# Performance work log

Measured on AMD Instinct MI355X. Metric: run time of the kernel, lower is better.

The kernel has to match this reference:

```python
import jax, jax.numpy as jnp
import numpy as np

D_MODEL = 1024
LAYER_IDX = 5
D_FF = 4096
SPARSITY = 0.9
TOKENS = 8192
IN_UP = D_MODEL * (LAYER_IDX + 1)  # 6144


def _sparse_weight(rng, out_f, in_f, sparsity):
    """Row-wise k-sparse weight matrix mimicking SparseLinear's padded-CSR:
    each output row keeps k = round(in_f*(1-sparsity)) live columns,
    values ~ U(-b, b) with b = 1/sqrt(effective_fan_in)."""
    k = max(1, round(in_f * (1.0 - sparsity)))
    bound = 1.0 / np.sqrt(max(1.0, in_f * (1.0 - sparsity)))
    scores = rng.random((out_f, in_f))
    # top-k per row -> boolean mask
    thresh = np.partition(scores, in_f - k, axis=1)[:, in_f - k][:, None]
    mask = scores >= thresh
    W = (rng.uniform(-bound, bound, (out_f, in_f)).astype(np.float32)) * mask
    return jnp.asarray(W), jnp.asarray(mask)


def setup_inputs() -> dict:
    key = jax.random.key(0)
    x = jax.random.normal(key, (TOKENS, IN_UP), dtype=jnp.float32)
    rng = np.random.default_rng(0)
    W_up, mask_up = _sparse_weight(rng, D_FF, IN_UP, SPARSITY)
    W_down, mask_down = _sparse_weight(rng, D_MODEL, D_FF, SPARSITY)
    return {"ffn_input_cat": x, "W_up": W_up, "W_down": W_down,
            "mask_up": mask_up, "mask_down": mask_down}


def reference(ffn_input_cat, W_up, W_down, mask_up, mask_down):
    # fc_down(gelu(fc_up(x))); SparseLinear == masked dense linear, no bias.
    # torch F.gelu default is the exact (erf) gelu.
    h = jax.nn.gelu(ffn_input_cat @ (W_up * mask_up).T, approximate=False)  # [T, d_ff]
    return h @ (W_down * mask_down).T  # [T, d_model]
```

## Files before the change

kernel.cpp:

```cpp
#include <hip/hip_runtime.h>
#include <cstdint>
#include <cstddef>

typedef unsigned short u16;
typedef __attribute__((ext_vector_type(8))) short  bf16x8;
typedef __attribute__((ext_vector_type(4))) float  f32x4;
typedef __attribute__((ext_vector_type(4))) unsigned short u16x4;

__device__ __forceinline__ u16 f2bf(float f) {
    unsigned u = __float_as_uint(f);
    unsigned r = (u + 0x7FFFu + ((u >> 16) & 1u)) >> 16;
    return (u16)r;
}

__device__ __forceinline__ void async_lds16(const u16* g, u16* l) {
    __builtin_amdgcn_global_load_lds(
        (const __attribute__((address_space(1))) unsigned int*)g,
        (__attribute__((address_space(3))) unsigned int*)l,
        16, 0, 0);
}

__global__ __launch_bounds__(256) void cvt3_kernel(const float* __restrict__ s0, u16* __restrict__ d0, int n0,
                                                   const float* __restrict__ s1, u16* __restrict__ d1, int n1,
                                                   const float* __restrict__ s2, u16* __restrict__ d2, int n2) {
    const int total = n0 + n1 + n2;
    for (int i = blockIdx.x * 256 + threadIdx.x; i < total; i += gridDim.x * 256) {
        const float* s; u16* d; int j = i;
        if (j < n0)            { s = s0; d = d0; }
        else if (j < n0 + n1)  { s = s1; d = d1; j -= n0; }
        else                   { s = s2; d = d2; j -= n0 + n1; }
        float4 a = ((const float4*)s)[j];
        u16x4 o;
        o[0] = f2bf(a.x); o[1] = f2bf(a.y); o[2] = f2bf(a.z); o[3] = f2bf(a.w);
        ((u16x4*)d)[j] = o;
    }
}

#define KSTEP 32
#define ASZ (256 * KSTEP)

template<bool GELU, typename OutT, int BN>
__global__ __launch_bounds__(512, 2) void gemm_ffn(const u16* __restrict__ A,
                                                   const u16* __restrict__ B,
                                                   OutT* __restrict__ C,
                                                   int K, int lda, int ldb, int ldc) {
    constexpr int NI = BN / 64;
    constexpr int SL = (BN == 256) ? 4 : 3;
    __shared__ __align__(16) u16 sA[4][ASZ];
    __shared__ __align__(16) u16 sB[4][BN * KSTEP];

    const int tid  = threadIdx.x;
    const int wave = tid >> 6;
    const int lane = tid & 63;
    const int quad = lane >> 4;
    const int r16  = lane & 15;

    const int nwg = gridDim.x * gridDim.y;
    int lin = blockIdx.y * gridDim.x + blockIdx.x;
    lin = (lin & 7) * (nwg >> 3) + (lin >> 3);
    const int n0 = (lin % gridDim.x) * BN;
    const int m0 = (lin / gridDim.x) * 256;

    const int wm = (wave >> 2) * 128;
    const int wn = (wave & 3) * (BN / 4);

    const int sr0 = wave * 16 + (lane >> 2);
    const int gc0 = (((lane & 3) ^ ((sr0 >> 1) & 3))) * 8;
    const int ldsw = wave * 512;

    const u16* gA0 = A + (size_t)(m0 + sr0) * lda + gc0;
    const u16* gA1 = gA0 + (size_t)128 * lda;
    const u16* gB0 = B + (size_t)(n0 + sr0) * ldb + gc0;
    const u16* gB1 = gB0 + (size_t)128 * ldb;

#define STAGE(kt, tb) { const int ko_ = (kt) * KSTEP; \
        async_lds16(gA0 + ko_, &sA[tb][ldsw]); \
        async_lds16(gA1 + ko_, &sA[tb][4096 + ldsw]); \
        async_lds16(gB0 + ko_, &sB[tb][ldsw]); \
        if constexpr (BN == 256) async_lds16(gB1 + ko_, &sB[tb][4096 + ldsw]); }

    int oA[8], oB[NI];
#pragma unroll
    for (int i = 0; i < 8; i++) {
        int ra = wm + i * 16 + r16;
        oA[i] = ra * 32 + ((quad ^ ((ra >> 1) & 3)) << 3);
    }
#pragma unroll
    for (int i = 0; i < NI; i++) {
        int rb = wn + i * 16 + r16;
        oB[i] = rb * 32 + ((quad ^ ((rb >> 1) & 3)) << 3);
    }

    f32x4 acc[8][NI] = {};
    const int NT = K / KSTEP;

#define LGKM0 asm volatile("s_waitcnt lgkmcnt(0)" ::: "memory"); __builtin_amdgcn_sched_barrier(0)
#define SBAR  __builtin_amdgcn_sched_barrier(0)
#define VMCNT_STEADY if constexpr (BN == 256) { asm volatile("s_waitcnt vmcnt(8)" ::: "memory"); } \
                     else { asm volatile("s_waitcnt vmcnt(6)" ::: "memory"); }
#define MFMA_Q(mb, AF, BF) \
    __builtin_amdgcn_s_setprio(1); \
    _Pragma("unroll") \
    for (int mi_ = 0; mi_ < 4; mi_++) \
        _Pragma("unroll") \
        for (int ni_ = 0; ni_ < NI; ni_++) \
            acc[(mb) + mi_][ni_] = __builtin_amdgcn_mfma_f32_16x16x32_bf16( \
                AF[mi_], BF[ni_], acc[(mb) + mi_][ni_], 0, 0, 0); \
    __builtin_amdgcn_s_setprio(0); \
    __builtin_amdgcn_sched_barrier(0)

    bf16x8 afA[4], afB[4], bfA[NI], bfB[NI];

    STAGE(0, 0); STAGE(1, 1); STAGE(2, 2);
    VMCNT_STEADY;
    __builtin_amdgcn_s_barrier();
    SBAR;
#pragma unroll
    for (int i = 0; i < 4; i++)  afA[i] = *(const bf16x8*)&sA[0][oA[i]];
#pragma unroll
    for (int i = 0; i < NI; i++) bfA[i] = *(const bf16x8*)&sB[0][oB[i]];
    LGKM0;

#define STEP(T, c, n1, t3, BC, BNx) { \
        int kt3_ = (T) + 3; if (kt3_ >= NT) kt3_ -= NT; \
        STAGE(kt3_, t3); \
        _Pragma("unroll") \
        for (int i = 0; i < 4; i++) afB[i] = *(const bf16x8*)&sA[c][oA[4 + i]]; \
        SBAR; \
        MFMA_Q(0, afA, BC); \
        LGKM0; \
        VMCNT_STEADY; \
        __builtin_amdgcn_s_barrier(); \
        SBAR; \
        _Pragma("unroll") \
        for (int i = 0; i < 4; i++)  afA[i] = *(const bf16x8*)&sA[n1][oA[i]]; \
        _Pragma("unroll") \
        for (int i = 0; i < NI; i++) BNx[i] = *(const bf16x8*)&sB[n1][oB[i]]; \
        SBAR; \
        MFMA_Q(4, afB, BC); \
        LGKM0; \
    }

    for (int t = 0; t < NT; t += 4) {
        STEP(t + 0, 0, 1, 3, bfA, bfB);
        STEP(t + 1, 1, 2, 0, bfB, bfA);
        STEP(t + 2, 2, 3, 1, bfA, bfB);
        STEP(t + 3, 3, 0, 2, bfB, bfA);
    }
    asm volatile("s_waitcnt vmcnt(0)" ::: "memory");

#pragma unroll
    for (int mi = 0; mi < 8; mi++) {
#pragma unroll
        for (int r = 0; r < 4; r++) {
            size_t rowoff = (size_t)(m0 + wm + mi * 16 + quad * 4 + r) * ldc;
#pragma unroll
            for (int ni = 0; ni < NI; ni++) {
                int col = n0 + wn + ni * 16 + r16;
                float v = acc[mi][ni][r];
                if constexpr (GELU)
                    v = 0.5f * v * (1.0f + erff(v * 0.70710678118654752f));
                if constexpr (sizeof(OutT) == 2)
                    ((u16*)C)[rowoff + col] = f2bf(v);
                else
                    ((float*)C)[rowoff + col] = v;
            }
        }
    }
}

extern "C" void kernel_launch(void* const* d_in, const int* in_sizes, int n_in,
                              void* d_out, int out_size, void* d_ws, size_t ws_size,
                              hipStream_t stream) {
    const int T   = 8192;
    const int DIN = 6144;
    const int DFF = 4096;
    const int DM  = 1024;

    const float* x  = (const float*)d_in[0];
    const float* wu = (const float*)d_in[1];
    const float* wd = (const float*)d_in[2];

    u16* xb  = (u16*)d_ws;
    u16* wub = xb  + (size_t)T * DIN;
    u16* wdb = wub + (size_t)DFF * DIN;
    u16* hb  = wdb + (size_t)DM * DFF;

    const int n4x  = T * DIN / 4;
    const int n4wu = DFF * DIN / 4;
    const int n4wd = DM * DFF / 4;
    cvt3_kernel<<<8192, 256, 0, stream>>>(x, xb, n4x, wu, wub, n4wu, wd, wdb, n4wd);

    dim3 g1(DFF / 256, T / 256);
    gemm_ffn<true, u16, 256><<<g1, 512, 0, stream>>>(xb, wub, hb, DIN, DIN, DIN, DFF);

    dim3 g2(DM / 128, T / 256);
    gemm_ffn<false, float, 128><<<g2, 512, 0, stream>>>(hb, wdb, (float*)d_out,
                                                        DFF, DFF, DFF, DM);
}
```

Measured before the change: 888.9 us.

## Restructure GEMM mainloop to double-buffered 64-wide K tiles with quadrant-split MFMA

```diff
diff --git a/kernel.cpp b/kernel.cpp
--- a/kernel.cpp
+++ b/kernel.cpp
@@ -36,18 +36,16 @@
     }
 }
 
-#define KSTEP 32
-#define ASZ (256 * KSTEP)
 
 template<bool GELU, typename OutT, int BN>
-__global__ __launch_bounds__(512, 2) void gemm_ffn(const u16* __restrict__ A,
-                                                   const u16* __restrict__ B,
-                                                   OutT* __restrict__ C,
-                                                   int K, int lda, int ldb, int ldc) {
-    constexpr int NI = BN / 64;
-    constexpr int SL = (BN == 256) ? 4 : 3;
-    __shared__ __align__(16) u16 sA[4][ASZ];
-    __shared__ __align__(16) u16 sB[4][BN * KSTEP];
+__global__ __launch_bounds__(512, 2) void gemm_q(const u16* __restrict__ A,
+                                                 const u16* __restrict__ B,
+                                                 OutT* __restrict__ C,
+                                                 int K, int lda, int ldb, int ldc) {
+    constexpr int NI  = BN / 64;
+    constexpr int NQN = NI / 2;
+    __shared__ __align__(16) u16 sA[2][256 * 64];
+    __shared__ __align__(16) u16 sB[2][BN * 64];
 
     const int tid  = threadIdx.x;
     const int wave = tid >> 6;
@@ -64,90 +62,88 @@
     const int wm = (wave >> 2) * 128;
     const int wn = (wave & 3) * (BN / 4);
 
-    const int sr0 = wave * 16 + (lane >> 2);
-    const int gc0 = (((lane & 3) ^ ((sr0 >> 1) & 3))) * 8;
-    const int ldsw = wave * 512;
+    const int srow = tid >> 3;
+    const int scol = (((tid & 7) ^ (srow & 7)) << 3);
+    const u16* gAs = A + (size_t)(m0 + srow) * lda + scol;
+    const u16* gBs = B + (size_t)(n0 + srow) * ldb + scol;
 
-    const u16* gA0 = A + (size_t)(m0 + sr0) * lda + gc0;
-    const u16* gA1 = gA0 + (size_t)128 * lda;
-    const u16* gB0 = B + (size_t)(n0 + sr0) * ldb + gc0;
-    const u16* gB1 = gB0 + (size_t)128 * ldb;
+#define STAGE_A(dst, kt) { const size_t ko_ = (size_t)(kt) * 64; \
+    _Pragma("unroll") for (int i_ = 0; i_ < 4; i_++) \
+        async_lds16(gAs + (size_t)(i_ * 64) * lda + ko_, (dst) + i_ * 4096 + tid * 8); }
+#define STAGE_B(dst, kt) { const size_t ko_ = (size_t)(kt) * 64; \
+    _Pragma("unroll") for (int i_ = 0; i_ < NI; i_++) \
+        async_lds16(gBs + (size_t)(i_ * 64) * ldb + ko_, (dst) + i_ * 4096 + tid * 8); }
 
-#define STAGE(kt, tb) { const int ko_ = (kt) * KSTEP; \
-        async_lds16(gA0 + ko_, &sA[tb][ldsw]); \
-        async_lds16(gA1 + ko_, &sA[tb][4096 + ldsw]); \
-        async_lds16(gB0 + ko_, &sB[tb][ldsw]); \
-        if constexpr (BN == 256) async_lds16(gB1 + ko_, &sB[tb][4096 + ldsw]); }
+    const int g0 = (quad ^ (r16 & 7)) << 3;
+    const int g1 = g0 ^ 32;
 
-    int oA[8], oB[NI];
-#pragma unroll
-    for (int i = 0; i < 8; i++) {
-        int ra = wm + i * 16 + r16;
-        oA[i] = ra * 32 + ((quad ^ ((ra >> 1) & 3)) << 3);
-    }
-#pragma unroll
-    for (int i = 0; i < NI; i++) {
-        int rb = wn + i * 16 + r16;
-        oB[i] = rb * 32 + ((quad ^ ((rb >> 1) & 3)) << 3);
-    }
+    struct FragT { bf16x8 a[4][2]; bf16x8 b[NQN][2]; };
 
-    f32x4 acc[8][NI] = {};
-    const int NT = K / KSTEP;
+#define READQ(F, Ab, Bb, qmi, qni) { \
+    _Pragma("unroll") for (int i_ = 0; i_ < 4; i_++) { \
+        const int ao_ = (wm + ((qmi) * 4 + i_) * 16 + r16) * 64; \
+        F.a[i_][0] = *(const bf16x8*)&(Ab)[ao_ + g0]; \
+        F.a[i_][1] = *(const bf16x8*)&(Ab)[ao_ + g1]; } \
+    _Pragma("unroll") for (int i_ = 0; i_ < NQN; i_++) { \
+        const int bo_ = (wn + ((qni) * NQN + i_) * 16 + r16) * 64; \
+        F.b[i_][0] = *(const bf16x8*)&(Bb)[bo_ + g0]; \
+        F.b[i_][1] = *(const bf16x8*)&(Bb)[bo_ + g1]; } }
 
 #define LGKM0 asm volatile("s_waitcnt lgkmcnt(0)" ::: "memory"); __builtin_amdgcn_sched_barrier(0)
-#define SBAR  __builtin_amdgcn_sched_barrier(0)
-#define VMCNT_STEADY if constexpr (BN == 256) { asm volatile("s_waitcnt vmcnt(8)" ::: "memory"); } \
-                     else { asm volatile("s_waitcnt vmcnt(6)" ::: "memory"); }
-#define MFMA_Q(mb, AF, BF) \
+#define VM0   asm volatile("s_waitcnt vmcnt(0)"  ::: "memory"); __builtin_amdgcn_sched_barrier(0)
+#define PIN   __builtin_amdgcn_sched_barrier(0)
+#define BARR  __builtin_amdgcn_s_barrier()
+
+#define MFMAQ(q, F) \
     __builtin_amdgcn_s_setprio(1); \
-    _Pragma("unroll") \
-    for (int mi_ = 0; mi_ < 4; mi_++) \
-        _Pragma("unroll") \
-        for (int ni_ = 0; ni_ < NI; ni_++) \
-            acc[(mb) + mi_][ni_] = __builtin_amdgcn_mfma_f32_16x16x32_bf16( \
-                AF[mi_], BF[ni_], acc[(mb) + mi_][ni_], 0, 0, 0); \
+    _Pragma("unroll") for (int mi_ = 0; mi_ < 4; mi_++) \
+    _Pragma("unroll") for (int ni_ = 0; ni_ < NQN; ni_++) { \
+        const int am_ = ((q) & 1) * 4 + mi_; \
+        const int an_ = ((q) >> 1) * NQN + ni_; \
+        acc[am_][an_] = __builtin_amdgcn_mfma_f32_16x16x32_bf16( \
+            F.a[mi_][0], F.b[ni_][0], acc[am_][an_], 0, 0, 0); \
+        acc[am_][an_] = __builtin_amdgcn_mfma_f32_16x16x32_bf16( \
+            F.a[mi_][1], F.b[ni_][1], acc[am_][an_], 0, 0, 0); } \
     __builtin_amdgcn_s_setprio(0); \
     __builtin_amdgcn_sched_barrier(0)
 
-    bf16x8 afA[4], afB[4], bfA[NI], bfB[NI];
+    f32x4 acc[8][NI] = {};
+    const int NT = K / 64;
 
-    STAGE(0, 0); STAGE(1, 1); STAGE(2, 2);
-    VMCNT_STEADY;
-    __builtin_amdgcn_s_barrier();
-    SBAR;
-#pragma unroll
-    for (int i = 0; i < 4; i++)  afA[i] = *(const bf16x8*)&sA[0][oA[i]];
-#pragma unroll
-    for (int i = 0; i < NI; i++) bfA[i] = *(const bf16x8*)&sB[0][oB[i]];
-    LGKM0;
+    FragT f0, f1;
 
-#define STEP(T, c, n1, t3, BC, BNx) { \
-        int kt3_ = (T) + 3; if (kt3_ >= NT) kt3_ -= NT; \
-        STAGE(kt3_, t3); \
-        _Pragma("unroll") \
-        for (int i = 0; i < 4; i++) afB[i] = *(const bf16x8*)&sA[c][oA[4 + i]]; \
-        SBAR; \
-        MFMA_Q(0, afA, BC); \
-        LGKM0; \
-        VMCNT_STEADY; \
-        __builtin_amdgcn_s_barrier(); \
-        SBAR; \
-        _Pragma("unroll") \
-        for (int i = 0; i < 4; i++)  afA[i] = *(const bf16x8*)&sA[n1][oA[i]]; \
-        _Pragma("unroll") \
-        for (int i = 0; i < NI; i++) BNx[i] = *(const bf16x8*)&sB[n1][oB[i]]; \
-        SBAR; \
-        MFMA_Q(4, afB, BC); \
-        LGKM0; \
+    STAGE_A(&sA[0][0], 0); STAGE_B(&sB[0][0], 0);
+    VM0;
+    BARR; PIN;
+    READQ(f0, sA[0], sB[0], 0, 0);
+
+    for (int t = 0; t < NT; ++t) {
+        const u16* Ac = sA[t & 1];
+        const u16* Bc = sB[t & 1];
+        u16* An = &sA[(t + 1) & 1][0];
+        u16* Bn = &sB[(t + 1) & 1][0];
+        const int kt = (t + 1 < NT) ? (t + 1) : 0;
+
+        READQ(f1, Ac, Bc, 1, 0);
+        STAGE_A(An, kt);
+        PIN; BARR; LGKM0;
+        MFMAQ(0, f0);
+
+        READQ(f0, Ac, Bc, 0, 1);
+        STAGE_B(Bn, kt);
+        PIN; BARR; LGKM0;
+        MFMAQ(1, f1);
+
+        READQ(f1, Ac, Bc, 1, 1);
+        PIN; BARR; LGKM0;
+        MFMAQ(2, f0);
+
+        VM0;
+        BARR; PIN;
+        if (t + 1 < NT) { READQ(f0, An, Bn, 0, 0); }
+        PIN;
+        MFMAQ(3, f1);
     }
-
-    for (int t = 0; t < NT; t += 4) {
-        STEP(t + 0, 0, 1, 3, bfA, bfB);
-        STEP(t + 1, 1, 2, 0, bfB, bfA);
-        STEP(t + 2, 2, 3, 1, bfA, bfB);
-        STEP(t + 3, 3, 0, 2, bfB, bfA);
-    }
-    asm volatile("s_waitcnt vmcnt(0)" ::: "memory");
 
 #pragma unroll
     for (int mi = 0; mi < 8; mi++) {
@@ -192,9 +188,9 @@
     cvt3_kernel<<<8192, 256, 0, stream>>>(x, xb, n4x, wu, wub, n4wu, wd, wdb, n4wd);
 
     dim3 g1(DFF / 256, T / 256);
-    gemm_ffn<true, u16, 256><<<g1, 512, 0, stream>>>(xb, wub, hb, DIN, DIN, DIN, DFF);
+    gemm_q<true, u16, 256><<<g1, 512, 0, stream>>>(xb, wub, hb, DIN, DIN, DIN, DFF);
 
     dim3 g2(DM / 128, T / 256);
-    gemm_ffn<false, float, 128><<<g2, 512, 0, stream>>>(hb, wdb, (float*)d_out,
-                                                        DFF, DFF, DFF, DM);
+    gemm_q<false, float, 128><<<g2, 512, 0, stream>>>(hb, wdb, (float*)d_out,
+                                                      DFF, DFF, DFF, DM);
 }
```

Result: slower. 953.8 us (+7.3%).
